# Optimization experiments

Hardware: AMD Instinct MI355X
Metric: run time of the kernel (lower is better)

The kernel has to match this reference:

```python
import jax, jax.numpy as jnp
import numpy as np

D = 768        # d_model
H = 12         # num_heads
HD = D // H    # head dim = 64
LAT = 256      # latent_dim
B = 16
S = 8192
ROPE_BASE = 10000.0


def get_alibi_slopes(n):
    # standard ALiBi geometric slopes for power-of-two-ish head counts
    start = 2.0 ** (-8.0 / n)
    return np.array([start ** (i + 1) for i in range(n)], dtype=np.float32)


def apply_rope(x, pos):
    # x: [B, L, H, HD], pos: [L] float positions
    half = HD // 2
    inv_freq = 1.0 / (ROPE_BASE ** (jnp.arange(0, half, dtype=jnp.float32) / half))
    ang = pos[:, None] * inv_freq                      # [L, half]
    cos = jnp.cos(ang)[None, :, None, :]               # [1, L, 1, half]
    sin = jnp.sin(ang)[None, :, None, :]
    x1, x2 = x[..., :half], x[..., half:]
    return jnp.concatenate([x1 * cos - x2 * sin, x1 * sin + x2 * cos], axis=-1)


def setup_inputs() -> dict:
    key = jax.random.key(0)
    ks = jax.random.split(key, 13)
    s = 1.0 / np.sqrt(D)
    return {
        "x": jax.random.normal(ks[0], (B, S, D), dtype=jnp.float32),
        "pool_token": jax.random.normal(ks[1], (1, 1, D), dtype=jnp.float32),
        "Wq": jax.random.normal(ks[2], (D, D), dtype=jnp.float32) * s,
        "bq": jnp.zeros((D,), dtype=jnp.float32),
        "Wk": jax.random.normal(ks[3], (D, D), dtype=jnp.float32) * s,
        "bk": jnp.zeros((D,), dtype=jnp.float32),
        "Wv": jax.random.normal(ks[4], (D, D), dtype=jnp.float32) * s,
        "bv": jnp.zeros((D,), dtype=jnp.float32),
        "Wo": jax.random.normal(ks[5], (D, D), dtype=jnp.float32) * s,
        "bo": jnp.zeros((D,), dtype=jnp.float32),
        "Wl": jax.random.normal(ks[6], (LAT, D), dtype=jnp.float32) * s,
        "bl": jnp.zeros((LAT,), dtype=jnp.float32),
    }


def reference(x, pool_token, Wq, bq, Wk, bk, Wv, bv, Wo, bo, Wl, bl):
    b = x.shape[0]
    memory = jnp.broadcast_to(pool_token, (b, 1, D))           # learned pooled query

    q = (memory @ Wq.T + bq).reshape(b, 1, H, HD)
    k = (x @ Wk.T + bk).reshape(b, S, H, HD)
    v = (x @ Wv.T + bv).reshape(b, S, H, HD)

    # RoPE: query sits at position 0, keys at positions 0..S-1
    q = apply_rope(q, jnp.zeros((1,), dtype=jnp.float32))
    k = apply_rope(k, jnp.arange(S, dtype=jnp.float32))

    scores = jnp.einsum("bqhd,bkhd->bhqk", q, k) / jnp.sqrt(jnp.float32(HD))  # [B,H,1,S]

    # ALiBi: linear penalty proportional to distance from the query (pos 0)
    slopes = jnp.asarray(get_alibi_slopes(H))                  # [H]
    bias = -slopes[:, None] * jnp.arange(S, dtype=jnp.float32)[None, :]       # [H,S]
    scores = scores + bias[None, :, None, :]

    attn = jax.nn.softmax(scores, axis=-1)                     # [B,H,1,S]
    out = jnp.einsum("bhqk,bkhd->bqhd", attn, v).reshape(b, 1, D)
    pooled = out @ Wo.T + bo                                   # [B,1,D]
    return pooled[:, 0] @ Wl.T + bl                            # [B,LAT]
```

## Files before the change

### kernel.cpp

```cpp
#include <hip/hip_runtime.h>

constexpr int DIM = 768;
constexpr int NH  = 12;
constexpr int HDm = 64;
constexpr int HALF = 32;
constexpr int LATm = 256;
constexpr int NB  = 16;
constexpr int SEQ = 8192;
constexpr int NPRIME = NH * DIM;
constexpr int SSPLIT = 16;
constexpr int SRANGE = SEQ / SSPLIT;

typedef short bf16x8 __attribute__((ext_vector_type(8)));
typedef float f32x4  __attribute__((ext_vector_type(4)));
using u16 = unsigned short;

__device__ __forceinline__ u16 f2b(float f) {
    unsigned int u = __float_as_uint(f);
    u += 0x7FFFu + ((u >> 16) & 1u);
    return (u16)(u >> 16);
}
__device__ __forceinline__ float b2f(u16 u) {
    union { unsigned int i; float f; } v; v.i = ((unsigned int)u) << 16; return v.f;
}

__global__ __launch_bounds__(256) void k_mv(const float* __restrict__ Wb,
        const float* __restrict__ bias, const float* __restrict__ vin,
        float* __restrict__ vout,
        int rows, int batch, int in_bstride, int out_bstride, int headslice) {
    int w = threadIdx.x >> 6, lane = threadIdx.x & 63;
    int gw = blockIdx.x * 4 + w;
    if (gw >= rows * batch) return;
    int b = gw / rows, row = gw - b * rows;
    const float* vi = vin + (size_t)b * in_bstride + (headslice ? (row >> 6) * DIM : 0);
    const float* wr = Wb + (size_t)row * DIM;
    float acc = 0.f;
    #pragma unroll
    for (int c = 0; c < DIM / 64; ++c)
        acc += wr[c * 64 + lane] * vi[c * 64 + lane];
    #pragma unroll
    for (int off = 32; off > 0; off >>= 1) acc += __shfl_xor(acc, off, 64);
    if (lane == 0) vout[(size_t)b * out_bstride + row] = acc + bias[row];
}

__global__ void k_uw(const float* __restrict__ q, const float* __restrict__ Wk,
                     u16* __restrict__ UWpT) {
    int tid = blockIdx.x * 256 + threadIdx.x;
    int np = tid >> 6, c = tid & 63;
    int h = np / DIM, d = np - h * DIM;
    int j = c & 31;
    float q1 = q[h * HDm + j], q2 = q[h * HDm + HALF + j];
    float wa = Wk[(size_t)(h * HDm + j) * DIM + d];
    float wb = Wk[(size_t)(h * HDm + HALF + j) * DIM + d];
    float v = (c < HALF) ? (q1 * wa + q2 * wb) : (q2 * wa - q1 * wb);
    UWpT[(size_t)np * 64 + c] = f2b(v * 0.125f);
}

__global__ void k_T(u16* __restrict__ T) {
    int tid = blockIdx.x * 256 + threadIdx.x;
    int s = tid >> 6, c = tid & 63;
    int j = c & 31;
    float f = expf(-(float)j * (9.210340372f / 32.f));
    float ang = (float)s * f;
    float v = (c < HALF) ? cosf(ang) : sinf(ang);
    T[tid] = f2b(v);
}

__global__ void k_eb(const float* __restrict__ q, const float* __restrict__ bk,
                     float* __restrict__ Ebias) {
    int tid = blockIdx.x * 256 + threadIdx.x;
    if (tid >= SEQ * NH) return;
    int s = tid / NH, h = tid - s * NH;
    float acc = 0.f;
    for (int j = 0; j < HALF; ++j) {
        float f = expf(-(float)j * (9.210340372f / 32.f));
        float sv, cv; sincosf((float)s * f, &sv, &cv);
        float b1 = bk[h * HDm + j], b2 = bk[h * HDm + HALF + j];
        float q1 = q[h * HDm + j], q2 = q[h * HDm + HALF + j];
        acc += cv * (q1 * b1 + q2 * b2) + sv * (q2 * b1 - q1 * b2);
    }
    Ebias[tid] = acc * 0.125f;
}

__global__ void __launch_bounds__(256) k_E(const u16* __restrict__ T,
        const u16* __restrict__ UWpT, u16* __restrict__ E, int s0) {
    int lane = threadIdx.x & 63, wid = threadIdx.x >> 6;
    int m0 = blockIdx.y * 128 + (wid >> 1) * 64;
    int n0 = blockIdx.x * 128 + (wid & 1) * 64;
    int l15 = lane & 15, quad = lane >> 4;
    f32x4 acc[4][4] = {};
    #pragma unroll
    for (int kq = 0; kq < 2; ++kq) {
        int kb = kq * 32 + quad * 8;
        bf16x8 a[4], b[4];
        #pragma unroll
        for (int i = 0; i < 4; ++i)
            a[i] = *(const bf16x8*)(T + (size_t)(s0 + m0 + i * 16 + l15) * 64 + kb);
        #pragma unroll
        for (int i = 0; i < 4; ++i)
            b[i] = *(const bf16x8*)(UWpT + (size_t)(n0 + i * 16 + l15) * 64 + kb);
        #pragma unroll
        for (int mi = 0; mi < 4; ++mi)
            #pragma unroll
            for (int ni = 0; ni < 4; ++ni)
                acc[mi][ni] = __builtin_amdgcn_mfma_f32_16x16x32_bf16(a[mi], b[ni], acc[mi][ni], 0, 0, 0);
    }
    #pragma unroll
    for (int mi = 0; mi < 4; ++mi)
        #pragma unroll
        for (int ni = 0; ni < 4; ++ni) {
            int col = n0 + ni * 16 + l15;
            #pragma unroll
            for (int r = 0; r < 4; ++r) {
                int row = m0 + mi * 16 + quad * 4 + r;
                E[(size_t)row * NPRIME + col] = f2b(acc[mi][ni][r]);
            }
        }
}

__global__ void __launch_bounds__(256) k_sc(const float* __restrict__ x,
        const u16* __restrict__ E, const float* __restrict__ Ebias,
        float* __restrict__ scores, int s0) {
    int lane = threadIdx.x & 63, wid = threadIdx.x >> 6;
    int sl = blockIdx.x * 4 + wid;
    int s = s0 + sl;
    int l15 = lane & 15, quad = lane >> 4;
    f32x4 acc = {};
    const float* xb = x + (size_t)l15 * SEQ * DIM + (size_t)s * DIM + quad * 8;
    const u16* eb = E + (size_t)sl * NPRIME + (size_t)l15 * DIM + quad * 8;
    #pragma unroll 4
    for (int kc = 0; kc < DIM / 32; ++kc) {
        float4 fa = *(const float4*)(xb + kc * 32);
        float4 fb = *(const float4*)(xb + kc * 32 + 4);
        bf16x8 av;
        av[0] = (short)f2b(fa.x); av[1] = (short)f2b(fa.y);
        av[2] = (short)f2b(fa.z); av[3] = (short)f2b(fa.w);
        av[4] = (short)f2b(fb.x); av[5] = (short)f2b(fb.y);
        av[6] = (short)f2b(fb.z); av[7] = (short)f2b(fb.w);
        bf16x8 bv = *(const bf16x8*)(eb + kc * 32);
        acc = __builtin_amdgcn_mfma_f32_16x16x32_bf16(av, bv, acc, 0, 0, 0);
    }
    int h = l15;
    if (h < NH) {
        float bias = Ebias[s * NH + h] - exp2f(-8.f * (h + 1) / 12.f) * (float)s;
        #pragma unroll
        for (int r = 0; r < 4; ++r) {
            int b = quad * 4 + r;
            scores[((size_t)b * NH + h) * SEQ + s] = acc[r] + bias;
        }
    }
}

__global__ void __launch_bounds__(256) k_sm(float* __restrict__ scores) {
    __shared__ float red[256];
    float* row = scores + (size_t)blockIdx.x * SEQ;
    int t = threadIdx.x;
    float m = -1e30f;
    for (int i = t; i < SEQ; i += 256) m = fmaxf(m, row[i]);
    red[t] = m; __syncthreads();
    for (int o = 128; o > 0; o >>= 1) { if (t < o) red[t] = fmaxf(red[t], red[t + o]); __syncthreads(); }
    m = red[0]; __syncthreads();
    float sum = 0.f;
    for (int i = t; i < SEQ; i += 256) sum += expf(row[i] - m);
    red[t] = sum; __syncthreads();
    for (int o = 128; o > 0; o >>= 1) { if (t < o) red[t] += red[t + o]; __syncthreads(); }
    float inv = 1.f / red[0];
    for (int i = t; i < SEQ; i += 256) row[i] = expf(row[i] - m) * inv;
}

__global__ void __launch_bounds__(256) k_pool(const float* __restrict__ x,
        const float* __restrict__ attn, float* __restrict__ part) {
    __shared__ float lds[12288];
    int bx = blockIdx.x;
    int sp = bx / 48, rem = bx % 48, b = rem / 3, dc = rem % 3;
    int s0 = sp * SRANGE, d0 = dc * 256;
    int t = threadIdx.x, dthr = t & 63, stripe = t >> 6;
    for (int i = t; i < NH * SRANGE; i += 256) {
        int h = i >> 9, si = i & 511;
        lds[i] = attn[((size_t)b * NH + h) * SEQ + s0 + si];
    }
    __syncthreads();
    float acc[NH][4] = {};
    const float* xp = x + ((size_t)b * SEQ + s0) * DIM + d0 + dthr * 4;
    for (int it = stripe * 128; it < stripe * 128 + 128; ++it) {
        float4 xv = *(const float4*)(xp + (size_t)it * DIM);
        #pragma unroll
        for (int h = 0; h < NH; ++h) {
            float a = lds[h * SRANGE + it];
            acc[h][0] += a * xv.x; acc[h][1] += a * xv.y;
            acc[h][2] += a * xv.z; acc[h][3] += a * xv.w;
        }
    }
    __syncthreads();
    #pragma unroll
    for (int h = 0; h < NH; ++h) {
        float* rp = lds + ((h * 4 + stripe) * 64 + dthr) * 4;
        rp[0] = acc[h][0]; rp[1] = acc[h][1]; rp[2] = acc[h][2]; rp[3] = acc[h][3];
    }
    __syncthreads();
    float* pb = part + (size_t)sp * (NB * NH * DIM) + (size_t)b * NH * DIM + d0;
    for (int i = t; i < NH * 64; i += 256) {
        int h = i >> 6, dt = i & 63;
        float4 v; v.x = v.y = v.z = v.w = 0.f;
        #pragma unroll
        for (int st = 0; st < 4; ++st) {
            const float* rp = lds + ((h * 4 + st) * 64 + dt) * 4;
            v.x += rp[0]; v.y += rp[1]; v.z += rp[2]; v.w += rp[3];
        }
        *(float4*)(pb + (size_t)h * DIM + dt * 4) = v;
    }
}

__global__ void k_red(const float* __restrict__ part, float* __restrict__ pooled) {
    int i = blockIdx.x * 256 + threadIdx.x;
    if (i < NB * NH * DIM) {
        float s = 0.f;
        for (int sp = 0; sp < SSPLIT; ++sp) s += part[(size_t)sp * (NB * NH * DIM) + i];
        pooled[i] = s;
    }
}

extern "C" void kernel_launch(void* const* d_in, const int* in_sizes, int n_in,
                              void* d_out, int out_size, void* d_ws, size_t ws_size,
                              hipStream_t stream) {
    (void)in_sizes; (void)n_in; (void)out_size;
    const float* x    = (const float*)d_in[0];
    const float* pool = (const float*)d_in[1];
    const float* Wq   = (const float*)d_in[2];
    const float* bq   = (const float*)d_in[3];
    const float* Wk   = (const float*)d_in[4];
    const float* bk   = (const float*)d_in[5];
    const float* Wv   = (const float*)d_in[6];
    const float* bv   = (const float*)d_in[7];
    const float* Wo   = (const float*)d_in[8];
    const float* bo   = (const float*)d_in[9];
    const float* Wl   = (const float*)d_in[10];
    const float* bl   = (const float*)d_in[11];

    char* w = (char*)d_ws;
    auto alloc = [&](size_t bytes) { char* p = w; w += (bytes + 255) & ~(size_t)255; return p; };
    float* q_f    = (float*)alloc(DIM * 4);
    u16*   UWpT   = (u16*)alloc((size_t)NPRIME * 64 * 2);
    u16*   Tt     = (u16*)alloc((size_t)SEQ * 64 * 2);
    float* Ebias  = (float*)alloc((size_t)SEQ * NH * 4);
    float* scores = (float*)alloc((size_t)NB * NH * SEQ * 4);
    float* part   = (float*)alloc((size_t)SSPLIT * NB * NH * DIM * 4);
    float* pooled = (float*)alloc((size_t)NB * NH * DIM * 4);
    float* o_buf  = (float*)alloc((size_t)NB * DIM * 4);
    float* p_buf  = (float*)alloc((size_t)NB * DIM * 4);

    size_t fixed_used = (size_t)(w - (char*)d_ws);
    size_t margin = 65536;
    size_t avail = (ws_size > fixed_used + margin) ? (ws_size - fixed_used - margin) : 0;
    size_t rows = avail / ((size_t)NPRIME * 2);
    int chunk = (rows >= (size_t)SEQ) ? SEQ : (int)(rows & ~(size_t)127);
    if (chunk < 128) chunk = 128;
    u16* E = (u16*)alloc((size_t)chunk * NPRIME * 2 + 8192);

    hipLaunchKernelGGL(k_mv, dim3(192), dim3(256), 0, stream,
                       Wq, bq, pool, q_f, DIM, 1, 0, DIM, 0);
    hipLaunchKernelGGL(k_uw, dim3(NPRIME * 64 / 256), dim3(256), 0, stream, q_f, Wk, UWpT);
    hipLaunchKernelGGL(k_T, dim3(SEQ * 64 / 256), dim3(256), 0, stream, Tt);
    hipLaunchKernelGGL(k_eb, dim3((SEQ * NH + 255) / 256), dim3(256), 0, stream, q_f, bk, Ebias);
    for (int s0 = 0; s0 < SEQ; s0 += chunk) {
        int cur = (SEQ - s0 < chunk) ? (SEQ - s0) : chunk;
        hipLaunchKernelGGL(k_E, dim3(NPRIME / 128, cur / 128), dim3(256), 0, stream,
                           Tt, UWpT, E, s0);
        hipLaunchKernelGGL(k_sc, dim3(cur / 4), dim3(256), 0, stream,
                           x, E, Ebias, scores, s0);
    }
    hipLaunchKernelGGL(k_sm, dim3(NB * NH), dim3(256), 0, stream, scores);
    hipLaunchKernelGGL(k_pool, dim3(SSPLIT * NB * 3), dim3(256), 0, stream, x, scores, part);
    hipLaunchKernelGGL(k_red, dim3((NB * NH * DIM + 255) / 256), dim3(256), 0, stream, part, pooled);
    hipLaunchKernelGGL(k_mv, dim3(NB * DIM / 4), dim3(256), 0, stream,
                       Wv, bv, pooled, o_buf, DIM, NB, NH * DIM, DIM, 1);
    hipLaunchKernelGGL(k_mv, dim3(NB * DIM / 4), dim3(256), 0, stream,
                       Wo, bo, o_buf, p_buf, DIM, NB, DIM, DIM, 0);
    hipLaunchKernelGGL(k_mv, dim3(NB * LATm / 4), dim3(256), 0, stream,
                       Wl, bl, p_buf, (float*)d_out, LATm, NB, DIM, LATm, 0);
}
```

Before: 778.4 us.

## Stage E tiles through LDS, split-K score blocks, async LDS loads in pooling

k_E now writes its output tile to shared memory and stores it with coalesced 16-byte rows instead of scattered 2-byte writes. k_sc gives each position its own block: the 16 batch rows of x are loaded into LDS with global_load_lds, the K dimension is split across the four waves, and the partial sums are reduced in LDS. k_sm uses 1024 threads per block. k_pool doubles its sequence split, double-buffers x tiles through async LDS loads, and accumulates in f32x4 registers. Together these raise memory coalescing and parallelism, at the cost of more partial-sum traffic in k_red and more LDS use per block.

```diff
diff --git a/kernel.cpp b/kernel.cpp
--- a/kernel.cpp
+++ b/kernel.cpp
@@ -8,8 +8,8 @@
 constexpr int NB  = 16;
 constexpr int SEQ = 8192;
 constexpr int NPRIME = NH * DIM;
-constexpr int SSPLIT = 16;
-constexpr int SRANGE = SEQ / SSPLIT;
+constexpr int PSP = 32;
+constexpr int PSR = SEQ / PSP;
 
 typedef short bf16x8 __attribute__((ext_vector_type(8)));
 typedef float f32x4  __attribute__((ext_vector_type(4)));
@@ -20,8 +20,11 @@
     u += 0x7FFFu + ((u >> 16) & 1u);
     return (u16)(u >> 16);
 }
-__device__ __forceinline__ float b2f(u16 u) {
-    union { unsigned int i; float f; } v; v.i = ((unsigned int)u) << 16; return v.f;
+
+__device__ __forceinline__ void gload_lds16(const void* g, void* l) {
+    __builtin_amdgcn_global_load_lds(
+        (const __attribute__((address_space(1))) unsigned int*)g,
+        (__attribute__((address_space(3))) unsigned int*)l, 16, 0, 0);
 }
 
 __global__ __launch_bounds__(256) void k_mv(const float* __restrict__ Wb,
@@ -84,6 +87,7 @@
 
 __global__ void __launch_bounds__(256) k_E(const u16* __restrict__ T,
         const u16* __restrict__ UWpT, u16* __restrict__ E, int s0) {
+    __shared__ u16 et[4 * 64 * 72];
     int lane = threadIdx.x & 63, wid = threadIdx.x >> 6;
     int m0 = blockIdx.y * 128 + (wid >> 1) * 64;
     int n0 = blockIdx.x * 128 + (wid & 1) * 64;
@@ -105,109 +109,162 @@
             for (int ni = 0; ni < 4; ++ni)
                 acc[mi][ni] = __builtin_amdgcn_mfma_f32_16x16x32_bf16(a[mi], b[ni], acc[mi][ni], 0, 0, 0);
     }
+    u16* ep = et + wid * (64 * 72);
     #pragma unroll
     for (int mi = 0; mi < 4; ++mi)
         #pragma unroll
         for (int ni = 0; ni < 4; ++ni) {
-            int col = n0 + ni * 16 + l15;
+            int col_l = ni * 16 + l15;
             #pragma unroll
             for (int r = 0; r < 4; ++r) {
-                int row = m0 + mi * 16 + quad * 4 + r;
-                E[(size_t)row * NPRIME + col] = f2b(acc[mi][ni][r]);
+                int row_l = mi * 16 + quad * 4 + r;
+                ep[row_l * 72 + col_l] = f2b(acc[mi][ni][r]);
             }
         }
+    #pragma unroll
+    for (int it = 0; it < 8; ++it) {
+        int row_l = it * 8 + (lane >> 3);
+        int cols  = (lane & 7) * 8;
+        bf16x8 v = *(const bf16x8*)&ep[row_l * 72 + cols];
+        *(bf16x8*)(E + (size_t)(m0 + row_l) * NPRIME + n0 + cols) = v;
+    }
 }
 
 __global__ void __launch_bounds__(256) k_sc(const float* __restrict__ x,
         const u16* __restrict__ E, const float* __restrict__ Ebias,
         float* __restrict__ scores, int s0) {
-    int lane = threadIdx.x & 63, wid = threadIdx.x >> 6;
-    int sl = blockIdx.x * 4 + wid;
-    int s = s0 + sl;
+    __shared__ float xt[16 * 772];
+    int t = threadIdx.x, lane = t & 63, w = t >> 6;
+    int sl = blockIdx.x;
+    int s  = s0 + sl;
     int l15 = lane & 15, quad = lane >> 4;
+
+    const u16* eb = E + (size_t)sl * NPRIME + (size_t)l15 * DIM + w * 6 * 32 + quad * 8;
+    bf16x8 bv[6];
+    #pragma unroll
+    for (int i = 0; i < 6; ++i) bv[i] = *(const bf16x8*)(eb + i * 32);
+
+    #pragma unroll
+    for (int i = 0; i < 12; ++i) {
+        int idx = w * 12 + i;
+        int tt = idx >> 4, b = idx & 15;
+        const char* g = (const char*)x + ((size_t)b * SEQ + s) * (DIM * 4) + tt * 1024 + (size_t)lane * 16;
+        char* l = (char*)xt + b * 3088 + tt * 1024;
+        gload_lds16(g, l);
+    }
+    asm volatile("s_waitcnt vmcnt(0)" ::: "memory");
+    __syncthreads();
+
     f32x4 acc = {};
-    const float* xb = x + (size_t)l15 * SEQ * DIM + (size_t)s * DIM + quad * 8;
-    const u16* eb = E + (size_t)sl * NPRIME + (size_t)l15 * DIM + quad * 8;
-    #pragma unroll 4
-    for (int kc = 0; kc < DIM / 32; ++kc) {
-        float4 fa = *(const float4*)(xb + kc * 32);
-        float4 fb = *(const float4*)(xb + kc * 32 + 4);
+    #pragma unroll
+    for (int i = 0; i < 6; ++i) {
+        int kc = w * 6 + i;
+        const float* xr = xt + l15 * 772 + kc * 32 + quad * 8;
+        float4 fa = *(const float4*)xr;
+        float4 fb = *(const float4*)(xr + 4);
         bf16x8 av;
         av[0] = (short)f2b(fa.x); av[1] = (short)f2b(fa.y);
         av[2] = (short)f2b(fa.z); av[3] = (short)f2b(fa.w);
         av[4] = (short)f2b(fb.x); av[5] = (short)f2b(fb.y);
         av[6] = (short)f2b(fb.z); av[7] = (short)f2b(fb.w);
-        bf16x8 bv = *(const bf16x8*)(eb + kc * 32);
-        acc = __builtin_amdgcn_mfma_f32_16x16x32_bf16(av, bv, acc, 0, 0, 0);
-    }
-    int h = l15;
-    if (h < NH) {
+        acc = __builtin_amdgcn_mfma_f32_16x16x32_bf16(av, bv[i], acc, 0, 0, 0);
+    }
+    __syncthreads();
+    f32x4* red = (f32x4*)xt;
+    red[w * 64 + lane] = acc;
+    __syncthreads();
+    if (t < NB * NH) {
+        int b = t / NH, h = t - b * NH;
+        int lr = (b >> 2) * 16 + h, r = b & 3;
+        float v = red[0 * 64 + lr][r] + red[1 * 64 + lr][r]
+                + red[2 * 64 + lr][r] + red[3 * 64 + lr][r];
         float bias = Ebias[s * NH + h] - exp2f(-8.f * (h + 1) / 12.f) * (float)s;
-        #pragma unroll
-        for (int r = 0; r < 4; ++r) {
-            int b = quad * 4 + r;
-            scores[((size_t)b * NH + h) * SEQ + s] = acc[r] + bias;
-        }
-    }
-}
-
-__global__ void __launch_bounds__(256) k_sm(float* __restrict__ scores) {
-    __shared__ float red[256];
+        scores[((size_t)b * NH + h) * SEQ + s] = v + bias;
+    }
+}
+
+__global__ void __launch_bounds__(1024) k_sm(float* __restrict__ scores) {
+    __shared__ float red[1024];
     float* row = scores + (size_t)blockIdx.x * SEQ;
     int t = threadIdx.x;
     float m = -1e30f;
-    for (int i = t; i < SEQ; i += 256) m = fmaxf(m, row[i]);
+    for (int i = t; i < SEQ; i += 1024) m = fmaxf(m, row[i]);
     red[t] = m; __syncthreads();
-    for (int o = 128; o > 0; o >>= 1) { if (t < o) red[t] = fmaxf(red[t], red[t + o]); __syncthreads(); }
+    for (int o = 512; o > 0; o >>= 1) { if (t < o) red[t] = fmaxf(red[t], red[t + o]); __syncthreads(); }
     m = red[0]; __syncthreads();
     float sum = 0.f;
-    for (int i = t; i < SEQ; i += 256) sum += expf(row[i] - m);
+    for (int i = t; i < SEQ; i += 1024) sum += expf(row[i] - m);
     red[t] = sum; __syncthreads();
-    for (int o = 128; o > 0; o >>= 1) { if (t < o) red[t] += red[t + o]; __syncthreads(); }
+    for (int o = 512; o > 0; o >>= 1) { if (t < o) red[t] += red[t + o]; __syncthreads(); }
     float inv = 1.f / red[0];
-    for (int i = t; i < SEQ; i += 256) row[i] = expf(row[i] - m) * inv;
+    for (int i = t; i < SEQ; i += 1024) row[i] = expf(row[i] - m) * inv;
 }
 
 __global__ void __launch_bounds__(256) k_pool(const float* __restrict__ x,
         const float* __restrict__ attn, float* __restrict__ part) {
-    __shared__ float lds[12288];
+    __shared__ float attn_s[12 * 256];
+    __shared__ float xbuf[2 * 16 * 256];
     int bx = blockIdx.x;
-    int sp = bx / 48, rem = bx % 48, b = rem / 3, dc = rem % 3;
-    int s0 = sp * SRANGE, d0 = dc * 256;
-    int t = threadIdx.x, dthr = t & 63, stripe = t >> 6;
-    for (int i = t; i < NH * SRANGE; i += 256) {
-        int h = i >> 9, si = i & 511;
-        lds[i] = attn[((size_t)b * NH + h) * SEQ + s0 + si];
-    }
+    int sp = bx / 48, rem = bx - sp * 48, b = rem / 3, dc = rem - (rem / 3) * 3;
+    int t = threadIdx.x, lane = t & 63, w = t >> 6;
+
+    for (int i = t; i < 12 * 256; i += 256)
+        attn_s[i] = attn[((size_t)b * NH + (i >> 8)) * SEQ + sp * PSR + (i & 255)];
+
+    auto stage = [&](int buf, int tt) {
+        #pragma unroll
+        for (int jj = 0; jj < 4; ++jj) {
+            int r = w * 4 + jj;
+            const char* g = (const char*)x
+                + (((size_t)b * SEQ + sp * PSR + tt * 16 + r) * DIM + dc * 256) * 4
+                + (size_t)lane * 16;
+            char* l = (char*)xbuf + buf * 16384 + r * 1024;
+            gload_lds16(g, l);
+        }
+    };
+
+    f32x4 acc[12] = {};
+    stage(0, 0);
+    asm volatile("s_waitcnt vmcnt(0)" ::: "memory");
     __syncthreads();
-    float acc[NH][4] = {};
-    const float* xp = x + ((size_t)b * SEQ + s0) * DIM + d0 + dthr * 4;
-    for (int it = stripe * 128; it < stripe * 128 + 128; ++it) {
-        float4 xv = *(const float4*)(xp + (size_t)it * DIM);
-        #pragma unroll
-        for (int h = 0; h < NH; ++h) {
-            float a = lds[h * SRANGE + it];
-            acc[h][0] += a * xv.x; acc[h][1] += a * xv.y;
-            acc[h][2] += a * xv.z; acc[h][3] += a * xv.w;
+    for (int tt = 0; tt < 16; ++tt) {
+        int cur = tt & 1;
+        if (tt < 15) stage(cur ^ 1, tt + 1);
+        const float* xb = xbuf + cur * 4096;
+        #pragma unroll
+        for (int j = 0; j < 4; ++j) {
+            int r = w * 4 + j;
+            float4 xv = *(const float4*)(xb + r * 256 + lane * 4);
+            int si = tt * 16 + r;
+            #pragma unroll
+            for (int h = 0; h < 12; ++h) {
+                float a = attn_s[h * 256 + si];
+                acc[h][0] += a * xv.x; acc[h][1] += a * xv.y;
+                acc[h][2] += a * xv.z; acc[h][3] += a * xv.w;
+            }
         }
-    }
-    __syncthreads();
-    #pragma unroll
-    for (int h = 0; h < NH; ++h) {
-        float* rp = lds + ((h * 4 + stripe) * 64 + dthr) * 4;
-        rp[0] = acc[h][0]; rp[1] = acc[h][1]; rp[2] = acc[h][2]; rp[3] = acc[h][3];
-    }
-    __syncthreads();
-    float* pb = part + (size_t)sp * (NB * NH * DIM) + (size_t)b * NH * DIM + d0;
-    for (int i = t; i < NH * 64; i += 256) {
-        int h = i >> 6, dt = i & 63;
-        float4 v; v.x = v.y = v.z = v.w = 0.f;
-        #pragma unroll
-        for (int st = 0; st < 4; ++st) {
-            const float* rp = lds + ((h * 4 + st) * 64 + dt) * 4;
-            v.x += rp[0]; v.y += rp[1]; v.z += rp[2]; v.w += rp[3];
+        asm volatile("s_waitcnt vmcnt(0)" ::: "memory");
+        __syncthreads();
+    }
+    float* red = xbuf;
+    #pragma unroll
+    for (int half = 0; half < 2; ++half) {
+        __syncthreads();
+        #pragma unroll
+        for (int hh = 0; hh < 6; ++hh)
+            *(f32x4*)(red + ((w * 64 + lane) * 6 + hh) * 4) = acc[half * 6 + hh];
+        __syncthreads();
+        for (int i = t; i < 6 * 64; i += 256) {
+            int hh = i >> 6, dt = i & 63;
+            f32x4 v = {};
+            #pragma unroll
+            for (int ww = 0; ww < 4; ++ww) {
+                f32x4 u = *(const f32x4*)(red + ((ww * 64 + dt) * 6 + hh) * 4);
+                v[0] += u[0]; v[1] += u[1]; v[2] += u[2]; v[3] += u[3];
+            }
+            *(f32x4*)(part + ((size_t)(sp * NB + b) * NH + half * 6 + hh) * DIM
+                      + dc * 256 + dt * 4) = v;
         }
-        *(float4*)(pb + (size_t)h * DIM + dt * 4) = v;
     }
 }
 
@@ -215,7 +272,7 @@
     int i = blockIdx.x * 256 + threadIdx.x;
     if (i < NB * NH * DIM) {
         float s = 0.f;
-        for (int sp = 0; sp < SSPLIT; ++sp) s += part[(size_t)sp * (NB * NH * DIM) + i];
+        for (int sp = 0; sp < PSP; ++sp) s += part[(size_t)sp * (NB * NH * DIM) + i];
         pooled[i] = s;
     }
 }
@@ -244,7 +301,7 @@
     u16*   Tt     = (u16*)alloc((size_t)SEQ * 64 * 2);
     float* Ebias  = (float*)alloc((size_t)SEQ * NH * 4);
     float* scores = (float*)alloc((size_t)NB * NH * SEQ * 4);
-    float* part   = (float*)alloc((size_t)SSPLIT * NB * NH * DIM * 4);
+    float* part   = (float*)alloc((size_t)PSP * NB * NH * DIM * 4);
     float* pooled = (float*)alloc((size_t)NB * NH * DIM * 4);
     float* o_buf  = (float*)alloc((size_t)NB * DIM * 4);
     float* p_buf  = (float*)alloc((size_t)NB * DIM * 4);
@@ -266,11 +323,11 @@
         int cur = (SEQ - s0 < chunk) ? (SEQ - s0) : chunk;
         hipLaunchKernelGGL(k_E, dim3(NPRIME / 128, cur / 128), dim3(256), 0, stream,
                            Tt, UWpT, E, s0);
-        hipLaunchKernelGGL(k_sc, dim3(cur / 4), dim3(256), 0, stream,
+        hipLaunchKernelGGL(k_sc, dim3(cur), dim3(256), 0, stream,
                            x, E, Ebias, scores, s0);
     }
-    hipLaunchKernelGGL(k_sm, dim3(NB * NH), dim3(256), 0, stream, scores);
-    hipLaunchKernelGGL(k_pool, dim3(SSPLIT * NB * 3), dim3(256), 0, stream, x, scores, part);
+    hipLaunchKernelGGL(k_sm, dim3(NB * NH), dim3(1024), 0, stream, scores);
+    hipLaunchKernelGGL(k_pool, dim3(PSP * NB * 3), dim3(256), 0, stream, x, scores, part);
     hipLaunchKernelGGL(k_red, dim3((NB * NH * DIM + 255) / 256), dim3(256), 0, stream, part, pooled);
     hipLaunchKernelGGL(k_mv, dim3(NB * DIM / 4), dim3(256), 0, stream,
                        Wv, bv, pooled, o_buf, DIM, NB, NH * DIM, DIM, 1);
```

After: 749.0 us. -3.8%, faster.
